# Kernel optimization log

Measured on AMD Instinct MI355X. Metric: run time of the kernel, lower is better.

The kernel has to match this reference:

```python
import jax, jax.numpy as jnp
import numpy as np
from jax import lax

HID = 96              # hidden_dim (C)
DM  = 2 * HID         # SS2D d_model (real+imag interleaved channels)
DI  = 2 * DM          # d_inner (expand=2, VMamba default)
N   = 16              # d_state
K   = 4               # scan directions
R   = (DM + 15) // 16 # dt_rank = ceil(d_model/16)
B_, H_, W_ = 1, 64, 64


def _layernorm(x, w, b, eps=1e-5):
    m = x.mean(-1, keepdims=True)
    v = ((x - m) ** 2).mean(-1, keepdims=True)
    return (x - m) * lax.rsqrt(v + eps) * w + b


def _selective_scan(xs, delta, A, Bs, Cs):
    # xs, delta: (B,K,D,L); A: (K,D,N); Bs, Cs: (B,K,N,L)
    def step(h, inp):
        dt, Bt, Ct, ut = inp                              # (B,K,D),(B,K,N),(B,K,N),(B,K,D)
        dA = jnp.exp(dt[..., None] * A[None])             # (B,K,D,N)
        h = h * dA + dt[..., None] * Bt[:, :, None, :] * ut[..., None]
        y = jnp.einsum('bkdn,bkn->bkd', h, Ct)
        return h, y
    inputs = (jnp.moveaxis(delta, -1, 0), jnp.moveaxis(Bs, -1, 0),
              jnp.moveaxis(Cs, -1, 0), jnp.moveaxis(xs, -1, 0))
    h0 = jnp.zeros(xs.shape[:3] + (N,), xs.dtype)
    _, ys = lax.scan(step, h0, inputs)                    # (L,B,K,D)
    return jnp.moveaxis(ys, 0, -1)                        # (B,K,D,L)


def _forward_core(x, x_proj_w, dt_w, dt_b, A_logs, Ds):
    # x: (B, DI, H, W) -- 4-direction cross-scan (VMamba SS2D)
    B, D, H, W = x.shape
    L = H * W
    x_hw = x.reshape(B, D, L)
    x_wh = x.transpose(0, 1, 3, 2).reshape(B, D, L)
    x_hwwh = jnp.stack([x_hw, x_wh], axis=1)                    # (B,2,D,L)
    xs = jnp.concatenate([x_hwwh, jnp.flip(x_hwwh, -1)], 1)     # (B,4,D,L)
    x_dbl = jnp.einsum('bkdl,kcd->bkcl', xs, x_proj_w)          # (B,K,R+2N,L)
    dts, Bs, Cs = jnp.split(x_dbl, [R, R + N], axis=2)
    dts = jnp.einsum('bkrl,kdr->bkdl', dts, dt_w)
    delta = jax.nn.softplus(dts + dt_b[None, :, :, None])
    A = -jnp.exp(A_logs.reshape(K, D, N))
    ys = _selective_scan(xs, delta, A, Bs, Cs)
    out_y = ys + Ds.reshape(K, D)[None, :, :, None] * xs        # (B,4,D,L)
    inv_y = jnp.flip(out_y[:, 2:4], -1)
    tr = lambda t: t.reshape(B, D, W, H).transpose(0, 1, 3, 2).reshape(B, D, L)
    y = out_y[:, 0] + inv_y[:, 0] + tr(out_y[:, 1]) + tr(inv_y[:, 1])
    return y.transpose(0, 2, 1).reshape(B, H, W, D)


def _ss2d(x, in_proj_w, conv_w, conv_b, x_proj_w, dt_w, dt_b,
          A_logs, Ds, out_norm_w, out_norm_b, out_proj_w):
    # x: (B, H, Wf, DM)
    xz = x @ in_proj_w.T                                        # (B,H,Wf,2*DI)
    xc, z = jnp.split(xz, 2, axis=-1)
    xc = xc.transpose(0, 3, 1, 2)                               # (B,DI,H,Wf)
    xc = lax.conv_general_dilated(xc, conv_w, (1, 1), 'SAME',
                                  feature_group_count=DI,
                                  dimension_numbers=('NCHW', 'OIHW', 'NCHW'))
    xc = jax.nn.silu(xc + conv_b[None, :, None, None])
    y = _forward_core(xc, x_proj_w, dt_w, dt_b, A_logs, Ds)     # (B,H,Wf,DI)
    y = _layernorm(y, out_norm_w, out_norm_b)
    y = y * jax.nn.silu(z)
    return y @ out_proj_w.T                                     # (B,H,Wf,DM)


def _freq_vss(x, in_proj_w, conv_w, conv_b, x_proj_w, dt_w, dt_b,
              A_logs, Ds, out_norm_w, out_norm_b, out_proj_w):
    B, H, W, C = x.shape
    xf = jnp.fft.rfft2(x, axes=(1, 2), norm='ortho')            # (B,H,Wf,C) complex
    Wf = xf.shape[2]
    # interleave real/imag into channels: (B,H,Wf,C,2) -> (B,H,Wf,2C)
    x1 = jnp.stack([xf.real, xf.imag], axis=4).reshape(B, H, Wf, 2 * C)
    att = _ss2d(x1, in_proj_w, conv_w, conv_b, x_proj_w, dt_w, dt_b,
                A_logs, Ds, out_norm_w, out_norm_b, out_proj_w)
    att = att.reshape(B, H, Wf, C, 2)
    attc = lax.complex(att[..., 0], att[..., 1])
    x1r = jnp.fft.irfft2(attc, s=(H, W), axes=(1, 2), norm='ortho')
    return x + x1r                                              # residual (drop_path=0)


def setup_inputs() -> dict:
    key = jax.random.key(0)
    ks = jax.random.split(key, 8)
    s = 0.02
    return {
        'x': jax.random.normal(ks[0], (B_, H_, W_, HID), jnp.float32),
        'in_proj_w': jax.random.normal(ks[1], (2 * DI, DM), jnp.float32) * s,
        'conv_w': jax.random.normal(ks[2], (DI, 1, 3, 3), jnp.float32) * s,
        'conv_b': jnp.zeros((DI,), jnp.float32),
        'x_proj_w': jax.random.normal(ks[3], (K, R + 2 * N, DI), jnp.float32) * s,
        'dt_w': jax.random.normal(ks[4], (K, DI, R), jnp.float32) * s,
        'dt_b': jax.random.normal(ks[5], (K, DI), jnp.float32) * 0.1,
        'A_logs': jnp.tile(jnp.log(jnp.arange(1, N + 1, dtype=jnp.float32))[None], (K * DI, 1)),
        'Ds': jnp.ones((K * DI,), jnp.float32),
        'out_norm_w': jnp.ones((DI,), jnp.float32),
        'out_norm_b': jnp.zeros((DI,), jnp.float32),
        'out_proj_w': jax.random.normal(ks[6], (DM, DI), jnp.float32) * s,
    }


def reference(x, in_proj_w, conv_w, conv_b, x_proj_w, dt_w, dt_b,
              A_logs, Ds, out_norm_w, out_norm_b, out_proj_w):
    return _freq_vss(x, in_proj_w, conv_w, conv_b, x_proj_w, dt_w, dt_b,
                     A_logs, Ds, out_norm_w, out_norm_b, out_proj_w)
```

## Files before the change

kernel.cpp:

```cpp
#include <hip/hip_runtime.h>
#include <hip/hip_bf16.h>

#define LQ   2112
#define DQ   384
#define NST  16
#define HQ   64
#define WFQ  33
#define CQ   96
#define SC   66
#define KDN  24576

#define AIPW  0
#define ACW   147456
#define ACB   150912
#define AXPW  151296
#define ADTW  218880
#define ADTB  237312
#define AANEG 238848
#define ADS   263424
#define ANW   264960
#define ANB   265344
#define AOPW  265728
#define ARTOT 339456

#define OFF_FFT   339456
#define OFF_XZ    744960
#define OFF_XCV   2366976
#define OFF_G     3177984
#define OFF_SUMDT 3549696
#define OFF_HEND  3651072
#define OFF_YS    5273088
#define OFF_YS4   6084096

#define P_ZR  0
#define P_ZI  202752

static __device__ __forceinline__ float u2f(unsigned short u)
{ union { unsigned int i; float f; } v; v.i = ((unsigned int)u) << 16; return v.f; }

static __device__ __forceinline__ float ldin(const void* p, int o, int isbf)
{
    if (isbf) return u2f(((const unsigned short*)p)[o]);
    return ((const float*)p)[o];
}

static __device__ __forceinline__ int isbf_of(const void* ds)
{ return (((const unsigned int*)ds)[0] == 0x3F803F80u) ? 1 : 0; }

__global__ __launch_bounds__(256) void k_cvt_rfftw(
    const void* __restrict__ x,   const void* __restrict__ ipw,
    const void* __restrict__ cw,  const void* __restrict__ cb,
    const void* __restrict__ xpw, const void* __restrict__ dtw,
    const void* __restrict__ dtb, const void* __restrict__ alog,
    const void* __restrict__ ds,  const void* __restrict__ nw,
    const void* __restrict__ nb,  const void* __restrict__ opw,
    float* __restrict__ arena, float* __restrict__ Zr, float* __restrict__ Zi)
{
    const int isbf = isbf_of(ds);
    if (blockIdx.x < 1326) {
        int t = blockIdx.x * 256 + threadIdx.x;
        int o = t;
        if (o < 147456) { arena[t] = ldin(ipw, o, isbf); return; }  o -= 147456;
        if (o < 3456)   { arena[t] = ldin(cw, o, isbf);  return; }  o -= 3456;
        if (o < 384)    { arena[t] = ldin(cb, o, isbf);  return; }  o -= 384;
        if (o < 67584)  { arena[t] = ldin(xpw, o, isbf); return; }  o -= 67584;
        if (o < 18432)  { arena[t] = ldin(dtw, o, isbf); return; }  o -= 18432;
        if (o < 1536)   { arena[t] = ldin(dtb, o, isbf); return; }  o -= 1536;
        if (o < 24576)  { arena[t] = -expf(ldin(alog, o, isbf)); return; }  o -= 24576;
        if (o < 1536)   { arena[t] = ldin(ds, o, isbf);  return; }  o -= 1536;
        if (o < 384)    { arena[t] = ldin(nw, o, isbf);  return; }  o -= 384;
        if (o < 384)    { arena[t] = ldin(nb, o, isbf);  return; }  o -= 384;
        arena[t] = ldin(opw, o, isbf);
        return;
    }
    __shared__ float tc[64], ts[64];
    if (threadIdx.x < 64) {
        float ang = -6.283185307179586f * (float)threadIdx.x / 64.f;
        float s, c; __sincosf(ang, &s, &c); tc[threadIdx.x] = c; ts[threadIdx.x] = s;
    }
    __syncthreads();
    int tid = (blockIdx.x - 1326) * 256 + threadIdx.x;
    int c = tid % CQ; int f = (tid / CQ) % WFQ; int h = tid / (CQ * WFQ);
    const int base = h * 64 * CQ + c;
    float zr = 0.f, zi = 0.f; int j = 0;
#pragma unroll 4
    for (int w = 0; w < 64; w++) {
        float xv = ldin(x, base + w * CQ, isbf);
        zr += xv * tc[j]; zi += xv * ts[j];
        j += f; j &= 63;
    }
    Zr[tid] = zr; Zi[tid] = zi;
}

__global__ __launch_bounds__(256) void k_ffth(const float* __restrict__ Zr, const float* __restrict__ Zi,
                                              float* __restrict__ x1)
{
    __shared__ float tc[64], ts[64];
    if (threadIdx.x < 64) {
        float ang = -6.283185307179586f * (float)threadIdx.x / 64.f;
        float s, c; __sincosf(ang, &s, &c); tc[threadIdx.x] = c; ts[threadIdx.x] = s;
    }
    __syncthreads();
    int tid = blockIdx.x * 256 + threadIdx.x;
    int c = tid % CQ; int f = (tid / CQ) % WFQ; int u = tid / (CQ * WFQ);
    float xr = 0.f, xi = 0.f; int j = 0;
    int base = f * CQ + c;
#pragma unroll 4
    for (int h = 0; h < 64; h++) {
        float zr = Zr[base + h * (WFQ * CQ)];
        float zi = Zi[base + h * (WFQ * CQ)];
        xr += zr * tc[j] - zi * ts[j];
        xi += zr * ts[j] + zi * tc[j];
        j += u; j &= 63;
    }
    int l = u * WFQ + f;
    x1[l * 192 + 2 * c]     = xr * (1.f / 64.f);
    x1[l * 192 + 2 * c + 1] = xi * (1.f / 64.f);
}

typedef __attribute__((ext_vector_type(8))) __bf16 bf16x8;
typedef __attribute__((ext_vector_type(4))) float f32x4;

__global__ __launch_bounds__(256) void k_gemm(const float* __restrict__ A, const float* __restrict__ W,
                                              float* __restrict__ C, int N, int K)
{
    __shared__ __bf16 Asm[64 * 40];
    __shared__ __bf16 Bsm[64 * 40];
    const int tid = threadIdx.x;
    const int bm = blockIdx.y * 64, bn = blockIdx.x * 64;
    const int wv = tid >> 6, lane = tid & 63;
    const int srow = tid >> 2, skk = (tid & 3) * 8;
    const int fm = lane & 15, fq = lane >> 4;
    f32x4 acc0 = {0.f, 0.f, 0.f, 0.f}, acc1 = acc0, acc2 = acc0, acc3 = acc0;
    const __bf16* afp = Asm + (wv * 16 + fm) * 40 + fq * 8;
    const __bf16* bfp = Bsm + fm * 40 + fq * 8;
    for (int k0 = 0; k0 < K; k0 += 32) {
        {
            const float* ap = A + (size_t)(bm + srow) * K + k0 + skk;
            float4 a0 = *(const float4*)ap, a1 = *(const float4*)(ap + 4);
            bf16x8 v = { (__bf16)a0.x, (__bf16)a0.y, (__bf16)a0.z, (__bf16)a0.w,
                         (__bf16)a1.x, (__bf16)a1.y, (__bf16)a1.z, (__bf16)a1.w };
            *(bf16x8*)(Asm + srow * 40 + skk) = v;
        }
        {
            float4 b0 = {0.f,0.f,0.f,0.f}, b1 = b0;
            if (bn + srow < N) {
                const float* wp = W + (size_t)(bn + srow) * K + k0 + skk;
                b0 = *(const float4*)wp; b1 = *(const float4*)(wp + 4);
            }
            bf16x8 v = { (__bf16)b0.x, (__bf16)b0.y, (__bf16)b0.z, (__bf16)b0.w,
                         (__bf16)b1.x, (__bf16)b1.y, (__bf16)b1.z, (__bf16)b1.w };
            *(bf16x8*)(Bsm + srow * 40 + skk) = v;
        }
        __syncthreads();
        bf16x8 af = *(const bf16x8*)afp;
        bf16x8 fb0 = *(const bf16x8*)(bfp);
        bf16x8 fb1 = *(const bf16x8*)(bfp + 16 * 40);
        bf16x8 fb2 = *(const bf16x8*)(bfp + 32 * 40);
        bf16x8 fb3 = *(const bf16x8*)(bfp + 48 * 40);
        acc0 = __builtin_amdgcn_mfma_f32_16x16x32_bf16(af, fb0, acc0, 0, 0, 0);
        acc1 = __builtin_amdgcn_mfma_f32_16x16x32_bf16(af, fb1, acc1, 0, 0, 0);
        acc2 = __builtin_amdgcn_mfma_f32_16x16x32_bf16(af, fb2, acc2, 0, 0, 0);
        acc3 = __builtin_amdgcn_mfma_f32_16x16x32_bf16(af, fb3, acc3, 0, 0, 0);
        __syncthreads();
    }
    const int m0 = bm + wv * 16 + fq * 4;
#pragma unroll
    for (int nt = 0; nt < 4; nt++) {
        f32x4 a = (nt == 0) ? acc0 : ((nt == 1) ? acc1 : ((nt == 2) ? acc2 : acc3));
        int n = bn + nt * 16 + fm;
        if (n < N) {
#pragma unroll
            for (int r = 0; r < 4; r++)
                C[(size_t)(m0 + r) * N + n] = a[r];
        }
    }
}

__global__ __launch_bounds__(256) void k_conv(const float* __restrict__ xz,
                                              const float* __restrict__ ar,
                                              float* __restrict__ xcv)
{
    int tid = blockIdx.x * 256 + threadIdx.x;
    int d = tid % DQ; int lp = tid / DQ;
    int l0 = lp * 2;
    float w9[9];
#pragma unroll
    for (int i = 0; i < 9; i++) w9[i] = ar[ACW + d * 9 + i];
    float cb = ar[ACB + d];
#pragma unroll
    for (int q = 0; q < 2; q++) {
        int l = l0 + q;
        int h = l / WFQ; int f = l % WFQ;
        float acc = cb;
#pragma unroll
        for (int ky = 0; ky < 3; ky++) {
            int hh = h + ky - 1;
            if (hh < 0 || hh >= HQ) continue;
#pragma unroll
            for (int kx = 0; kx < 3; kx++) {
                int ff = f + kx - 1;
                if (ff < 0 || ff >= WFQ) continue;
                acc += w9[ky * 3 + kx] * xz[(size_t)(hh * WFQ + ff) * 768 + d];
            }
        }
        float sig = 1.f / (1.f + __expf(-acc));
        xcv[(size_t)l * DQ + d] = acc * sig;
    }
}

static __device__ __forceinline__ float softplus_f(float a)
{
    return (a > 15.f) ? a : __logf(1.f + __expf(a));
}

template<int KK> static __device__ __forceinline__ int chunk_l0(int s)
{
    if (KK == 0) return s * 32;
    if (KK == 1) return (s & 1) * 1056 + (s >> 1);
    if (KK == 2) return 2111 - s * 32;
    return 2111 - (s & 1) * 1056 - (s >> 1);
}
template<int KK> static __device__ __forceinline__ int chunk_stp()
{
    if (KK == 0) return 1;
    if (KK == 1) return 33;
    if (KK == 2) return -1;
    return -33;
}

template<int KK, int PASS2> static __device__ __forceinline__ void scan_body(
    const float* __restrict__ xcv, const float* __restrict__ G, const float* __restrict__ ar,
    float* __restrict__ hend, float* __restrict__ sumdt, float* __restrict__ ys4)
{
    const int s = blockIdx.x, db = blockIdx.y;
    const int lane = threadIdx.x;
    const int stp = chunk_stp<KK>();
    const int l0 = chunk_l0<KK>(s);
    const int kd = KK * DQ + db * 64 + lane;

    const float* wp = ar + ADTW + kd * 12;
    const float4 wA = *(const float4*)(wp);
    const float4 wB = *(const float4*)(wp + 4);
    const float4 wC = *(const float4*)(wp + 8);
    const float bias = ar[ADTB + kd];
    const float* ap = ar + AANEG + kd * 16;
    const float4 Av0 = *(const float4*)(ap);
    const float4 Av1 = *(const float4*)(ap + 4);
    const float4 Av2 = *(const float4*)(ap + 8);
    const float4 Av3 = *(const float4*)(ap + 12);

    float4 h0 = make_float4(0.f, 0.f, 0.f, 0.f), h1 = h0, h2 = h0, h3 = h0;
    if (PASS2) {
        const float* hp = hend + (size_t)s * KDN + kd * 16;
        h0 = *(const float4*)(hp);
        h1 = *(const float4*)(hp + 4);
        h2 = *(const float4*)(hp + 8);
        h3 = *(const float4*)(hp + 12);
    }

    float* ysk = ys4 + (size_t)KK * (LQ * DQ);
    float sd_acc = 0.f;
    for (int i = 0; i < 32; i++) {
        const int lt = l0 + stp * i;
        const float* gr = G + (size_t)lt * 176 + KK * 44;
        float4 g0 = *(const float4*)(gr);
        float4 g1 = *(const float4*)(gr + 4);
        float4 g2 = *(const float4*)(gr + 8);
        float u = xcv[(size_t)lt * DQ + db * 64 + lane];
        float acc = bias
            + wA.x * g0.x + wA.y * g0.y + wA.z * g0.z + wA.w * g0.w
            + wB.x * g1.x + wB.y * g1.y + wB.z * g1.z + wB.w * g1.w
            + wC.x * g2.x + wC.y * g2.y + wC.z * g2.z + wC.w * g2.w;
        float dt = softplus_f(acc);
        float du = dt * u;
        float4 b0 = *(const float4*)(gr + 12);
        float4 b1 = *(const float4*)(gr + 16);
        float4 b2 = *(const float4*)(gr + 20);
        float4 b3 = *(const float4*)(gr + 24);
        h0.x = h0.x * __expf(dt * Av0.x) + du * b0.x;
        h0.y = h0.y * __expf(dt * Av0.y) + du * b0.y;
        h0.z = h0.z * __expf(dt * Av0.z) + du * b0.z;
        h0.w = h0.w * __expf(dt * Av0.w) + du * b0.w;
        h1.x = h1.x * __expf(dt * Av1.x) + du * b1.x;
        h1.y = h1.y * __expf(dt * Av1.y) + du * b1.y;
        h1.z = h1.z * __expf(dt * Av1.z) + du * b1.z;
        h1.w = h1.w * __expf(dt * Av1.w) + du * b1.w;
        h2.x = h2.x * __expf(dt * Av2.x) + du * b2.x;
        h2.y = h2.y * __expf(dt * Av2.y) + du * b2.y;
        h2.z = h2.z * __expf(dt * Av2.z) + du * b2.z;
        h2.w = h2.w * __expf(dt * Av2.w) + du * b2.w;
        h3.x = h3.x * __expf(dt * Av3.x) + du * b3.x;
        h3.y = h3.y * __expf(dt * Av3.y) + du * b3.y;
        h3.z = h3.z * __expf(dt * Av3.z) + du * b3.z;
        h3.w = h3.w * __expf(dt * Av3.w) + du * b3.w;
        if (PASS2) {
            float4 c0 = *(const float4*)(gr + 28);
            float4 c1 = *(const float4*)(gr + 32);
            float4 c2 = *(const float4*)(gr + 36);
            float4 c3 = *(const float4*)(gr + 40);
            float y0 = h0.x * c0.x + h0.y * c0.y + h0.z * c0.z + h0.w * c0.w;
            float y1 = h1.x * c1.x + h1.y * c1.y + h1.z * c1.z + h1.w * c1.w;
            float y2 = h2.x * c2.x + h2.y * c2.y + h2.z * c2.z + h2.w * c2.w;
            float y3 = h3.x * c3.x + h3.y * c3.y + h3.z * c3.z + h3.w * c3.w;
            ysk[(size_t)lt * DQ + db * 64 + lane] = (y0 + y1) + (y2 + y3);
        } else {
            sd_acc += dt;
        }
    }

    if (!PASS2) {
        float* hp = hend + (size_t)s * KDN + kd * 16;
        *(float4*)(hp)      = h0;
        *(float4*)(hp + 4)  = h1;
        *(float4*)(hp + 8)  = h2;
        *(float4*)(hp + 12) = h3;
        sumdt[s * 1536 + kd] = sd_acc;
    }
}

__global__ __launch_bounds__(64) void k_scan1(const float* __restrict__ xcv, const float* __restrict__ G,
                                              const float* __restrict__ ar,
                                              float* __restrict__ hend, float* __restrict__ sumdt,
                                              float* __restrict__ ys4)
{
    switch (blockIdx.z) {
        case 0: scan_body<0, 0>(xcv, G, ar, hend, sumdt, ys4); break;
        case 1: scan_body<1, 0>(xcv, G, ar, hend, sumdt, ys4); break;
        case 2: scan_body<2, 0>(xcv, G, ar, hend, sumdt, ys4); break;
        default: scan_body<3, 0>(xcv, G, ar, hend, sumdt, ys4); break;
    }
}

__global__ __launch_bounds__(64) void k_scan2(const float* __restrict__ xcv, const float* __restrict__ G,
                                              const float* __restrict__ ar,
                                              float* __restrict__ hend, float* __restrict__ sumdt,
                                              float* __restrict__ ys4)
{
    switch (blockIdx.z) {
        case 0: scan_body<0, 1>(xcv, G, ar, hend, sumdt, ys4); break;
        case 1: scan_body<1, 1>(xcv, G, ar, hend, sumdt, ys4); break;
        case 2: scan_body<2, 1>(xcv, G, ar, hend, sumdt, ys4); break;
        default: scan_body<3, 1>(xcv, G, ar, hend, sumdt, ys4); break;
    }
}

__global__ __launch_bounds__(256) void k_comb(const float* __restrict__ ar, const float* __restrict__ sumdt,
                                              float* __restrict__ hend)
{
    int tid = blockIdx.x * 256 + threadIdx.x;
    int kd = tid >> 4;
    float Av = ar[AANEG + tid];
    float hbuf[6], sbuf[6];
#pragma unroll
    for (int q = 0; q < 6; q++) {
        hbuf[q] = hend[(size_t)q * KDN + tid];
        sbuf[q] = sumdt[q * 1536 + kd];
    }
    float hp = 0.f;
    for (int s = 0; s < SC; s += 6) {
        float hc[6], sc6[6];
#pragma unroll
        for (int q = 0; q < 6; q++) { hc[q] = hbuf[q]; sc6[q] = sbuf[q]; }
#pragma unroll
        for (int q = 0; q < 6; q++) {
            int sn = s + 6 + q;
            if (sn < SC) {
                hbuf[q] = hend[(size_t)sn * KDN + tid];
                sbuf[q] = sumdt[sn * 1536 + kd];
            }
        }
#pragma unroll
        for (int q = 0; q < 6; q++) {
            hend[(size_t)(s + q) * KDN + tid] = hp;
            hp = hp * __expf(Av * sc6[q]) + hc[q];
        }
    }
}

__global__ __launch_bounds__(128) void k_lnmul(const float* __restrict__ ys4, const float* __restrict__ xcv,
                                               const float* __restrict__ xz, const float* __restrict__ ar,
                                               float* __restrict__ ym)
{
    int l = blockIdx.x; int tid = threadIdx.x;
    float v[3]; float s1 = 0.f, s2 = 0.f;
#pragma unroll
    for (int j = 0; j < 3; j++) {
        int d = tid + j * 128;
        size_t idx = (size_t)l * DQ + d;
        float sd = ar[ADS + d] + ar[ADS + DQ + d] + ar[ADS + 2 * DQ + d] + ar[ADS + 3 * DQ + d];
        float a = ys4[idx] + ys4[811008 + idx] + ys4[1622016 + idx] + ys4[2433024 + idx]
                + sd * xcv[idx];
        v[j] = a; s1 += a; s2 += a * a;
    }
#pragma unroll
    for (int off = 1; off < 64; off <<= 1) { s1 += __shfl_xor(s1, off); s2 += __shfl_xor(s2, off); }
    __shared__ float sh[4];
    if ((tid & 63) == 0) { sh[(tid >> 6) * 2] = s1; sh[(tid >> 6) * 2 + 1] = s2; }
    __syncthreads();
    s1 = sh[0] + sh[2]; s2 = sh[1] + sh[3];
    float m = s1 * (1.f / 384.f);
    float var = s2 * (1.f / 384.f) - m * m;
    float rs = rsqrtf(var + 1e-5f);
#pragma unroll
    for (int j = 0; j < 3; j++) {
        int d = tid + j * 128;
        float z = xz[(size_t)l * 768 + 384 + d];
        float sig = 1.f / (1.f + __expf(-z));
        ym[(size_t)l * DQ + d] = ((v[j] - m) * rs * ar[ANW + d] + ar[ANB + d]) * (z * sig);
    }
}

__global__ __launch_bounds__(256) void k_iffth(const float* __restrict__ att,
                                               float* __restrict__ Yr, float* __restrict__ Yi)
{
    __shared__ float tc[64], ts[64];
    if (threadIdx.x < 64) {
        float ang = 6.283185307179586f * (float)threadIdx.x / 64.f;
        float s, c; __sincosf(ang, &s, &c); tc[threadIdx.x] = c; ts[threadIdx.x] = s;
    }
    __syncthreads();
    int tid = blockIdx.x * 256 + threadIdx.x;
    int c = tid % CQ; int f = (tid / CQ) % WFQ; int hp = tid / (CQ * WFQ);
    float yr = 0.f, yi = 0.f; int j = 0;
#pragma unroll 4
    for (int h = 0; h < 64; h++) {
        const float* ap = att + (size_t)(h * WFQ + f) * 192 + 2 * c;
        float arv = ap[0], aiv = ap[1];
        yr += arv * tc[j] - aiv * ts[j];
        yi += arv * ts[j] + aiv * tc[j];
        j += hp; j &= 63;
    }
    Yr[tid] = yr * 0.125f;
    Yi[tid] = yi * 0.125f;
}

__global__ __launch_bounds__(256) void k_irfft_res(const float* __restrict__ Yr, const float* __restrict__ Yi,
                                                   const void* __restrict__ x, const void* __restrict__ ds,
                                                   void* __restrict__ out)
{
    __shared__ float tc[64], ts[64];
    if (threadIdx.x < 64) {
        float ang = 6.283185307179586f * (float)threadIdx.x / 64.f;
        float s, c; __sincosf(ang, &s, &c); tc[threadIdx.x] = c; ts[threadIdx.x] = s;
    }
    __syncthreads();
    const int isbf = isbf_of(ds);
    int tid = blockIdx.x * 256 + threadIdx.x;
    int c = tid % CQ; int w = (tid / CQ) % 64; int h = tid / (CQ * 64);
    const float* yr = Yr + h * (WFQ * CQ) + c;
    const float* yi = Yi + h * (WFQ * CQ) + c;
    float acc = yr[0];
    acc += ((w & 1) ? -1.f : 1.f) * yr[32 * CQ];
    float a2 = 0.f; int j = w & 63;
#pragma unroll 4
    for (int f = 1; f < 32; f++) {
        a2 += yr[f * CQ] * tc[j] - yi[f * CQ] * ts[j];
        j += w; j &= 63;
    }
    acc += 2.f * a2;
    float val = ldin(x, tid, isbf) + 0.125f * acc;
    if (isbf) ((__hip_bfloat16*)out)[tid] = __float2bfloat16(val);
    else      ((float*)out)[tid] = val;
}

extern "C" void kernel_launch(void* const* d_in, const int* in_sizes, int n_in,
                              void* d_out, int out_size, void* d_ws, size_t ws_size,
                              hipStream_t stream)
{
    float* ws    = (float*)d_ws;
    float* ar    = ws;
    float* Zr    = ws + OFF_FFT + P_ZR;
    float* Zi    = ws + OFF_FFT + P_ZI;
    float* xz    = ws + OFF_XZ;
    float* xcv   = ws + OFF_XCV;
    float* G     = ws + OFF_G;
    float* sumdt = ws + OFF_SUMDT;
    float* hend  = ws + OFF_HEND;
    float* x1    = ws + OFF_YS;
    float* ys4   = ws + OFF_YS4;

    float* ym   = hend;
    float* att  = xcv;

    k_cvt_rfftw<<<2118, 256, 0, stream>>>(d_in[0], d_in[1], d_in[2], d_in[3], d_in[4], d_in[5],
                                          d_in[6], d_in[7], d_in[8], d_in[9], d_in[10], d_in[11],
                                          ar, Zr, Zi);
    k_ffth<<<792, 256, 0, stream>>>(Zr, Zi, x1);
    k_gemm<<<dim3(12, 33), 256, 0, stream>>>(x1, ar + AIPW, xz, 768, 192);
    k_conv<<<1584, 256, 0, stream>>>(xz, ar, xcv);
    k_gemm<<<dim3(3, 33), 256, 0, stream>>>(xcv, ar + AXPW, G, 176, 384);
    k_scan1<<<dim3(SC, 6, 4), 64, 0, stream>>>(xcv, G, ar, hend, sumdt, ys4);
    k_comb<<<96, 256, 0, stream>>>(ar, sumdt, hend);
    k_scan2<<<dim3(SC, 6, 4), 64, 0, stream>>>(xcv, G, ar, hend, sumdt, ys4);
    k_lnmul<<<LQ, 128, 0, stream>>>(ys4, xcv, xz, ar, ym);
    k_gemm<<<dim3(3, 33), 256, 0, stream>>>(ym, ar + AOPW, att, 192, 384);
    k_iffth<<<792, 256, 0, stream>>>(att, Zr, Zi);
    k_irfft_res<<<1536, 256, 0, stream>>>(Zr, Zi, d_in[0], d_in[8], d_out);
}
```

Baseline: 211.1 us.

## Feed GEMMs pre-converted bf16 operands and interleave complex FFT buffers

Producer kernels (weight conversion, row FFT, conv, layernorm-mul) now also write bf16 copies of GEMM operands, so the GEMM loads bf16 directly instead of loading fp32 and converting on every tile. The separate real and imaginary FFT planes are merged into float2 arrays so each complex value is fetched with one load. This is meant to cut GEMM load traffic and conversion work. In exchange it adds extra bf16 stores and a larger workspace layout.

```diff
diff --git a/kernel.cpp b/kernel.cpp
--- a/kernel.cpp
+++ b/kernel.cpp
@@ -23,17 +23,23 @@
 #define AOPW  265728
 #define ARTOT 339456
 
-#define OFF_FFT   339456
-#define OFF_XZ    744960
-#define OFF_XCV   2366976
-#define OFF_G     3177984
-#define OFF_SUMDT 3549696
-#define OFF_HEND  3651072
-#define OFF_YS    5273088
-#define OFF_YS4   6084096
-
-#define P_ZR  0
-#define P_ZI  202752
+#define ABIP     339456
+#define BXP_OFF  147456
+#define BOP_OFF  215040
+
+#define OFF_FFT   483840
+#define OFF_XZ    889344
+#define OFF_XCV   2511360
+#define OFF_XCVB  3322368
+#define OFF_G     3727872
+#define OFF_SUMDT 4099584
+#define OFF_HEND  4200960
+#define OFF_YS    5822976
+#define OFF_YS4   6228480
+
+typedef __attribute__((ext_vector_type(8))) __bf16 bf16x8;
+typedef __attribute__((ext_vector_type(2))) __bf16 bf16x2;
+typedef __attribute__((ext_vector_type(4))) float f32x4;
 
 static __device__ __forceinline__ float u2f(unsigned short u)
 { union { unsigned int i; float f; } v; v.i = ((unsigned int)u) << 16; return v.f; }
@@ -54,23 +60,26 @@
     const void* __restrict__ dtb, const void* __restrict__ alog,
     const void* __restrict__ ds,  const void* __restrict__ nw,
     const void* __restrict__ nb,  const void* __restrict__ opw,
-    float* __restrict__ arena, float* __restrict__ Zr, float* __restrict__ Zi)
+    float* __restrict__ arena, float2* __restrict__ Zc)
 {
     const int isbf = isbf_of(ds);
+    __bf16* bw = (__bf16*)(arena + ABIP);
     if (blockIdx.x < 1326) {
         int t = blockIdx.x * 256 + threadIdx.x;
         int o = t;
-        if (o < 147456) { arena[t] = ldin(ipw, o, isbf); return; }  o -= 147456;
+        if (o < 147456) { float v = ldin(ipw, o, isbf); arena[t] = v; bw[o] = (__bf16)v; return; }
+        o -= 147456;
         if (o < 3456)   { arena[t] = ldin(cw, o, isbf);  return; }  o -= 3456;
         if (o < 384)    { arena[t] = ldin(cb, o, isbf);  return; }  o -= 384;
-        if (o < 67584)  { arena[t] = ldin(xpw, o, isbf); return; }  o -= 67584;
+        if (o < 67584)  { float v = ldin(xpw, o, isbf); arena[t] = v; bw[BXP_OFF + o] = (__bf16)v; return; }
+        o -= 67584;
         if (o < 18432)  { arena[t] = ldin(dtw, o, isbf); return; }  o -= 18432;
         if (o < 1536)   { arena[t] = ldin(dtb, o, isbf); return; }  o -= 1536;
         if (o < 24576)  { arena[t] = -expf(ldin(alog, o, isbf)); return; }  o -= 24576;
         if (o < 1536)   { arena[t] = ldin(ds, o, isbf);  return; }  o -= 1536;
         if (o < 384)    { arena[t] = ldin(nw, o, isbf);  return; }  o -= 384;
         if (o < 384)    { arena[t] = ldin(nb, o, isbf);  return; }  o -= 384;
-        arena[t] = ldin(opw, o, isbf);
+        { float v = ldin(opw, o, isbf); arena[t] = v; bw[BOP_OFF + o] = (__bf16)v; }
         return;
     }
     __shared__ float tc[64], ts[64];
@@ -89,11 +98,10 @@
         zr += xv * tc[j]; zi += xv * ts[j];
         j += f; j &= 63;
     }
-    Zr[tid] = zr; Zi[tid] = zi;
-}
-
-__global__ __launch_bounds__(256) void k_ffth(const float* __restrict__ Zr, const float* __restrict__ Zi,
-                                              float* __restrict__ x1)
+    Zc[tid] = make_float2(zr, zi);
+}
+
+__global__ __launch_bounds__(256) void k_ffth(const float2* __restrict__ Zc, __bf16* __restrict__ x1b)
 {
     __shared__ float tc[64], ts[64];
     if (threadIdx.x < 64) {
@@ -107,21 +115,17 @@
     int base = f * CQ + c;
 #pragma unroll 4
     for (int h = 0; h < 64; h++) {
-        float zr = Zr[base + h * (WFQ * CQ)];
-        float zi = Zi[base + h * (WFQ * CQ)];
-        xr += zr * tc[j] - zi * ts[j];
-        xi += zr * ts[j] + zi * tc[j];
+        float2 z = Zc[base + h * (WFQ * CQ)];
+        xr += z.x * tc[j] - z.y * ts[j];
+        xi += z.x * ts[j] + z.y * tc[j];
         j += u; j &= 63;
     }
     int l = u * WFQ + f;
-    x1[l * 192 + 2 * c]     = xr * (1.f / 64.f);
-    x1[l * 192 + 2 * c + 1] = xi * (1.f / 64.f);
-}
-
-typedef __attribute__((ext_vector_type(8))) __bf16 bf16x8;
-typedef __attribute__((ext_vector_type(4))) float f32x4;
-
-__global__ __launch_bounds__(256) void k_gemm(const float* __restrict__ A, const float* __restrict__ W,
+    bf16x2 v = { (__bf16)(xr * (1.f / 64.f)), (__bf16)(xi * (1.f / 64.f)) };
+    *(bf16x2*)(x1b + l * 192 + 2 * c) = v;
+}
+
+__global__ __launch_bounds__(256) void k_gemm(const __bf16* __restrict__ A, const __bf16* __restrict__ W,
                                               float* __restrict__ C, int N, int K)
 {
     __shared__ __bf16 Asm[64 * 40];
@@ -135,21 +139,13 @@
     const __bf16* afp = Asm + (wv * 16 + fm) * 40 + fq * 8;
     const __bf16* bfp = Bsm + fm * 40 + fq * 8;
     for (int k0 = 0; k0 < K; k0 += 32) {
+        *(bf16x8*)(Asm + srow * 40 + skk) =
+            *(const bf16x8*)(A + (size_t)(bm + srow) * K + k0 + skk);
         {
-            const float* ap = A + (size_t)(bm + srow) * K + k0 + skk;
-            float4 a0 = *(const float4*)ap, a1 = *(const float4*)(ap + 4);
-            bf16x8 v = { (__bf16)a0.x, (__bf16)a0.y, (__bf16)a0.z, (__bf16)a0.w,
-                         (__bf16)a1.x, (__bf16)a1.y, (__bf16)a1.z, (__bf16)a1.w };
-            *(bf16x8*)(Asm + srow * 40 + skk) = v;
-        }
-        {
-            float4 b0 = {0.f,0.f,0.f,0.f}, b1 = b0;
-            if (bn + srow < N) {
-                const float* wp = W + (size_t)(bn + srow) * K + k0 + skk;
-                b0 = *(const float4*)wp; b1 = *(const float4*)(wp + 4);
-            }
-            bf16x8 v = { (__bf16)b0.x, (__bf16)b0.y, (__bf16)b0.z, (__bf16)b0.w,
-                         (__bf16)b1.x, (__bf16)b1.y, (__bf16)b1.z, (__bf16)b1.w };
+            bf16x8 v = { (__bf16)0.f, (__bf16)0.f, (__bf16)0.f, (__bf16)0.f,
+                         (__bf16)0.f, (__bf16)0.f, (__bf16)0.f, (__bf16)0.f };
+            if (bn + srow < N)
+                v = *(const bf16x8*)(W + (size_t)(bn + srow) * K + k0 + skk);
             *(bf16x8*)(Bsm + srow * 40 + skk) = v;
         }
         __syncthreads();
@@ -179,7 +175,7 @@
 
 __global__ __launch_bounds__(256) void k_conv(const float* __restrict__ xz,
                                               const float* __restrict__ ar,
-                                              float* __restrict__ xcv)
+                                              float* __restrict__ xcv, __bf16* __restrict__ xcvb)
 {
     int tid = blockIdx.x * 256 + threadIdx.x;
     int d = tid % DQ; int lp = tid / DQ;
@@ -205,7 +201,9 @@
             }
         }
         float sig = 1.f / (1.f + __expf(-acc));
-        xcv[(size_t)l * DQ + d] = acc * sig;
+        float val = acc * sig;
+        xcv[(size_t)l * DQ + d] = val;
+        xcvb[(size_t)l * DQ + d] = (__bf16)val;
     }
 }
 
@@ -380,7 +378,7 @@
 
 __global__ __launch_bounds__(128) void k_lnmul(const float* __restrict__ ys4, const float* __restrict__ xcv,
                                                const float* __restrict__ xz, const float* __restrict__ ar,
-                                               float* __restrict__ ym)
+                                               __bf16* __restrict__ ymb)
 {
     int l = blockIdx.x; int tid = threadIdx.x;
     float v[3]; float s1 = 0.f, s2 = 0.f;
@@ -407,12 +405,11 @@
         int d = tid + j * 128;
         float z = xz[(size_t)l * 768 + 384 + d];
         float sig = 1.f / (1.f + __expf(-z));
-        ym[(size_t)l * DQ + d] = ((v[j] - m) * rs * ar[ANW + d] + ar[ANB + d]) * (z * sig);
-    }
-}
-
-__global__ __launch_bounds__(256) void k_iffth(const float* __restrict__ att,
-                                               float* __restrict__ Yr, float* __restrict__ Yi)
+        ymb[(size_t)l * DQ + d] = (__bf16)(((v[j] - m) * rs * ar[ANW + d] + ar[ANB + d]) * (z * sig));
+    }
+}
+
+__global__ __launch_bounds__(256) void k_iffth(const float* __restrict__ att, float2* __restrict__ Yc)
 {
     __shared__ float tc[64], ts[64];
     if (threadIdx.x < 64) {
@@ -431,11 +428,10 @@
         yi += arv * ts[j] + aiv * tc[j];
         j += hp; j &= 63;
     }
-    Yr[tid] = yr * 0.125f;
-    Yi[tid] = yi * 0.125f;
-}
-
-__global__ __launch_bounds__(256) void k_irfft_res(const float* __restrict__ Yr, const float* __restrict__ Yi,
+    Yc[tid] = make_float2(yr * 0.125f, yi * 0.125f);
+}
+
+__global__ __launch_bounds__(256) void k_irfft_res(const float2* __restrict__ Yc,
                                                    const void* __restrict__ x, const void* __restrict__ ds,
                                                    void* __restrict__ out)
 {
@@ -448,14 +444,15 @@
     const int isbf = isbf_of(ds);
     int tid = blockIdx.x * 256 + threadIdx.x;
     int c = tid % CQ; int w = (tid / CQ) % 64; int h = tid / (CQ * 64);
-    const float* yr = Yr + h * (WFQ * CQ) + c;
-    const float* yi = Yi + h * (WFQ * CQ) + c;
-    float acc = yr[0];
-    acc += ((w & 1) ? -1.f : 1.f) * yr[32 * CQ];
+    const float2* yc = Yc + h * (WFQ * CQ) + c;
+    float2 y0 = yc[0];
+    float acc = y0.x;
+    acc += ((w & 1) ? -1.f : 1.f) * yc[32 * CQ].x;
     float a2 = 0.f; int j = w & 63;
 #pragma unroll 4
     for (int f = 1; f < 32; f++) {
-        a2 += yr[f * CQ] * tc[j] - yi[f * CQ] * ts[j];
+        float2 yf = yc[f * CQ];
+        a2 += yf.x * tc[j] - yf.y * ts[j];
         j += w; j &= 63;
     }
     acc += 2.f * a2;
@@ -470,31 +467,33 @@
 {
     float* ws    = (float*)d_ws;
     float* ar    = ws;
-    float* Zr    = ws + OFF_FFT + P_ZR;
-    float* Zi    = ws + OFF_FFT + P_ZI;
+    __bf16* bw   = (__bf16*)(ws + ABIP);
+    float2* Zc   = (float2*)(ws + OFF_FFT);
     float* xz    = ws + OFF_XZ;
     float* xcv   = ws + OFF_XCV;
+    __bf16* xcvb = (__bf16*)(ws + OFF_XCVB);
     float* G     = ws + OFF_G;
     float* sumdt = ws + OFF_SUMDT;
     float* hend  = ws + OFF_HEND;
-    float* x1    = ws + OFF_YS;
+    __bf16* x1b  = (__bf16*)(ws + OFF_YS);
     float* ys4   = ws + OFF_YS4;
 
-    float* ym   = hend;
+    __bf16* ymb = (__bf16*)hend;
     float* att  = xcv;
+    float2* Yc  = Zc;
 
     k_cvt_rfftw<<<2118, 256, 0, stream>>>(d_in[0], d_in[1], d_in[2], d_in[3], d_in[4], d_in[5],
                                           d_in[6], d_in[7], d_in[8], d_in[9], d_in[10], d_in[11],
-                                          ar, Zr, Zi);
-    k_ffth<<<792, 256, 0, stream>>>(Zr, Zi, x1);
-    k_gemm<<<dim3(12, 33), 256, 0, stream>>>(x1, ar + AIPW, xz, 768, 192);
-    k_conv<<<1584, 256, 0, stream>>>(xz, ar, xcv);
-    k_gemm<<<dim3(3, 33), 256, 0, stream>>>(xcv, ar + AXPW, G, 176, 384);
+                                          ar, Zc);
+    k_ffth<<<792, 256, 0, stream>>>(Zc, x1b);
+    k_gemm<<<dim3(12, 33), 256, 0, stream>>>(x1b, bw, xz, 768, 192);
+    k_conv<<<1584, 256, 0, stream>>>(xz, ar, xcv, xcvb);
+    k_gemm<<<dim3(3, 33), 256, 0, stream>>>(xcvb, bw + BXP_OFF, G, 176, 384);
     k_scan1<<<dim3(SC, 6, 4), 64, 0, stream>>>(xcv, G, ar, hend, sumdt, ys4);
     k_comb<<<96, 256, 0, stream>>>(ar, sumdt, hend);
     k_scan2<<<dim3(SC, 6, 4), 64, 0, stream>>>(xcv, G, ar, hend, sumdt, ys4);
-    k_lnmul<<<LQ, 128, 0, stream>>>(ys4, xcv, xz, ar, ym);
-    k_gemm<<<dim3(3, 33), 256, 0, stream>>>(ym, ar + AOPW, att, 192, 384);
-    k_iffth<<<792, 256, 0, stream>>>(att, Zr, Zi);
-    k_irfft_res<<<1536, 256, 0, stream>>>(Zr, Zi, d_in[0], d_in[8], d_out);
-}
+    k_lnmul<<<LQ, 128, 0, stream>>>(ys4, xcv, xz, ar, ymb);
+    k_gemm<<<dim3(3, 33), 256, 0, stream>>>(ymb, bw + BOP_OFF, att, 192, 384);
+    k_iffth<<<792, 256, 0, stream>>>(att, Yc);
+    k_irfft_res<<<1536, 256, 0, stream>>>(Yc, d_in[0], d_in[8], d_out);
+}
```

Result: faster. 202.0 us (-4.3%).
